# Optimization experiments

Measured on AMD Instinct MI355X. Metric: run time of the kernel, lower is better.

## Reference

```python
import jax, jax.numpy as jnp
import numpy as np

BIN_RES = 0.01
NUM_BINS = 512
T0 = 0.0
DECAY = 2.0
SCALE = 0.05
N = 131072


def setup_inputs() -> dict:
    key = jax.random.key(0)
    k1, k2, k3, k4, k5, k6 = jax.random.split(key, 6)
    means = jax.random.normal(k1, (N, 3), dtype=jnp.float32)
    scan_point = jax.random.normal(k2, (3,), dtype=jnp.float32)
    # parameters initialized near their nn.Parameter defaults with small noise
    colours = 0.1 + 0.05 * jax.random.normal(k3, (N, 1), dtype=jnp.float32)
    coefficients = 0.1 * jax.random.normal(k4, (N, 1), dtype=jnp.float32)
    opacities = 0.1 * jax.random.normal(k5, (N, 1), dtype=jnp.float32)
    pre_act_scales = jnp.log(jnp.float32(SCALE)) + 0.1 * jax.random.normal(k6, (N, 1), dtype=jnp.float32)
    return {
        "means": means,
        "scan_point": scan_point,
        "colours": colours,
        "coefficients": coefficients,
        "opacities": opacities,
        "pre_act_scales": pre_act_scales,
        "view_id": 0,
    }


def reference(means, scan_point, colours, coefficients, opacities, pre_act_scales, view_id):
    # render_conf_hist2 (confocal=True path)
    intensity = jax.nn.sigmoid(opacities[:, view_id]) * (colours[:, 0] ** 2)  # [N]
    coeff = jax.nn.sigmoid(coefficients)  # [N,1]
    r0 = jnp.linalg.norm(means - scan_point[None, :], axis=1, keepdims=True)  # [N,1]
    r_ = T0 / 2 + (BIN_RES / 2) * jnp.arange(1, 1 + NUM_BINS, dtype=jnp.float32)  # [B]
    r = r_[None, :]  # [1,B]
    sigma = jnp.mean(jnp.exp(pre_act_scales), axis=1, keepdims=True)  # [N,1]
    sigma = jnp.clip(sigma, BIN_RES / 2)  # lower clip only
    d = r - r0  # [N,B]
    g = jnp.exp(-0.5 * (d / sigma) ** 2)  # [N,B]
    pdf1 = np.sqrt(0.5 / np.pi) * g / sigma
    pdf2 = d * g / (sigma ** 2)
    pdf = coeff * pdf1 + (1.0 - coeff) * pdf2
    pr = jnp.clip(pdf * (BIN_RES / 2), 0.0, 1.0)  # [N,B]
    hist = jnp.sum(intensity[:, None] * pr, axis=0)  # [B]
    hist = hist / jnp.power(r_, DECAY)
    return hist
```

## Files before the change

### kernel.cpp

```cpp
#include <hip/hip_runtime.h>
#include <math.h>

#define NBINS 512
#define K1_THREADS 512

__global__ __launch_bounds__(K1_THREADS) void gauss_scatter_fused(
    const float* __restrict__ means,
    const float* __restrict__ scan_point,
    const float* __restrict__ colours,
    const float* __restrict__ coefficients,
    const float* __restrict__ opacities,
    const float* __restrict__ pre_act,
    const int*   __restrict__ view_id_p,
    float* __restrict__ out,
    int n)
{
    __shared__ float hist[NBINS];
    const int tid = threadIdx.x;
    hist[tid] = 0.0f;
    __syncthreads();

    const int i = blockIdx.x * K1_THREADS + tid;
    if (i < n) {
        const int vid = view_id_p[0];
        const float op  = opacities[i + vid];
        const float col = colours[i];
        const float inten = (1.0f / (1.0f + __expf(-op))) * col * col;
        const float cf    = 1.0f / (1.0f + __expf(-coefficients[i]));

        const float dx = means[3*i]   - scan_point[0];
        const float dy = means[3*i+1] - scan_point[1];
        const float dz = means[3*i+2] - scan_point[2];
        const float r0 = sqrtf(fmaf(dx, dx, fmaf(dy, dy, dz*dz)));

        const float sigma = fmaxf(__expf(pre_act[i]), 0.005f);

        const float q  = 0.8493218002880191f / sigma;
        const float c  = inten * 0.005f;
        const float A2 = c * cf * 0.3989422804014327f / sigma;
        const float B3 = c * (1.0f - cf) / (0.8493218002880191f * sigma);

        const float rlo = r0 - (cf / (1.0f - cf)) * 0.3989422804014327f * sigma;
        const float rhi = r0 + 7.5f * sigma;
        int blo = (int)ceilf(rlo * 200.0f - 1.0f);
        int bhi = (int)floorf(rhi * 200.0f - 1.0f);
        blo = max(blo, 0);
        bhi = min(bhi, NBINS - 1);

        float e = (0.005f * (float)(blo + 1) - r0) * q;
        const float de = 0.005f * q;
        for (int b = blo; b <= bhi; ++b) {
            const float g = __builtin_amdgcn_exp2f(-(e * e));
            const float t = g * fmaf(B3, e, A2);
            unsafeAtomicAdd(&hist[b], t);
            e += de;
        }
    }
    __syncthreads();

    const float v = hist[tid];
    if (v != 0.0f) {
        const float r = 0.005f * (float)(tid + 1);
        unsafeAtomicAdd(&out[tid], v / (r * r));
    }
}

extern "C" void kernel_launch(void* const* d_in, const int* in_sizes, int n_in,
                              void* d_out, int out_size, void* d_ws, size_t ws_size,
                              hipStream_t stream) {
    const float* means        = (const float*)d_in[0];
    const float* scan_point   = (const float*)d_in[1];
    const float* colours      = (const float*)d_in[2];
    const float* coefficients = (const float*)d_in[3];
    const float* opacities    = (const float*)d_in[4];
    const float* pre_act      = (const float*)d_in[5];
    const int*   view_id      = (const int*)d_in[6];

    const int n = in_sizes[2];
    const int G = (n + K1_THREADS - 1) / K1_THREADS;

    float* out = (float*)d_out;

    hipMemsetAsync(out, 0, NBINS * sizeof(float), stream);

    gauss_scatter_fused<<<G, K1_THREADS, 0, stream>>>(
        means, scan_point, colours, coefficients, opacities, pre_act,
        view_id, out, n);
}
```

Baseline: 23.63 us.

## Replace global atomics and memset with cooperative grid-sync reduction

Switches to a persistent cooperative launch of 256 blocks, each grid-striding over gaussians and accumulating into a shared histogram. Each block writes its partial histogram to workspace, then after a grid-wide sync the blocks reduce the partials per bin with wave shuffles. This removes the separate memset launch and the global atomic contention on the output. In exchange it adds a grid barrier, a workspace round trip, and the overhead of a cooperative launch.

```diff
diff --git a/kernel.cpp b/kernel.cpp
--- a/kernel.cpp
+++ b/kernel.cpp
@@ -1,10 +1,14 @@
 #include <hip/hip_runtime.h>
+#include <hip/hip_cooperative_groups.h>
 #include <math.h>
 
-#define NBINS 512
-#define K1_THREADS 512
+namespace cg = cooperative_groups;
 
-__global__ __launch_bounds__(K1_THREADS) void gauss_scatter_fused(
+#define NBINS  512
+#define TPB    512
+#define GBLKS  256
+
+__global__ __launch_bounds__(TPB) void gauss_fused_coop(
     const float* __restrict__ means,
     const float* __restrict__ scan_point,
     const float* __restrict__ colours,
@@ -12,6 +16,7 @@
     const float* __restrict__ opacities,
     const float* __restrict__ pre_act,
     const int*   __restrict__ view_id_p,
+    float* __restrict__ partial,
     float* __restrict__ out,
     int n)
 {
@@ -20,8 +25,7 @@
     hist[tid] = 0.0f;
     __syncthreads();
 
-    const int i = blockIdx.x * K1_THREADS + tid;
-    if (i < n) {
+    for (int i = blockIdx.x * TPB + tid; i < n; i += GBLKS * TPB) {
         const int vid = view_id_p[0];
         const float op  = opacities[i + vid];
         const float col = colours[i];
@@ -58,10 +62,28 @@
     }
     __syncthreads();
 
-    const float v = hist[tid];
-    if (v != 0.0f) {
+    {
         const float r = 0.005f * (float)(tid + 1);
-        unsafeAtomicAdd(&out[tid], v / (r * r));
+        partial[blockIdx.x * NBINS + tid] = hist[tid] / (r * r);
+    }
+    __threadfence();
+    cg::this_grid().sync();
+
+    const int half = tid >> 8;
+    const int bin  = blockIdx.x * 2 + half;
+    const int g    = tid & 255;
+    float s = partial[g * NBINS + bin];
+
+    #pragma unroll
+    for (int off = 32; off > 0; off >>= 1)
+        s += __shfl_down(s, off, 64);
+
+    __shared__ float wsum[8];
+    if ((tid & 63) == 0) wsum[tid >> 6] = s;
+    __syncthreads();
+    if ((tid & 255) == 0) {
+        const int base = half * 4;
+        out[bin] = wsum[base] + wsum[base + 1] + wsum[base + 2] + wsum[base + 3];
     }
 }
 
@@ -76,14 +98,15 @@
     const float* pre_act      = (const float*)d_in[5];
     const int*   view_id      = (const int*)d_in[6];
 
-    const int n = in_sizes[2];
-    const int G = (n + K1_THREADS - 1) / K1_THREADS;
+    int n = in_sizes[2];
+    float* partial = (float*)d_ws;
+    float* out     = (float*)d_out;
 
-    float* out = (float*)d_out;
-
-    hipMemsetAsync(out, 0, NBINS * sizeof(float), stream);
-
-    gauss_scatter_fused<<<G, K1_THREADS, 0, stream>>>(
-        means, scan_point, colours, coefficients, opacities, pre_act,
-        view_id, out, n);
+    void* args[] = {
+        (void*)&means, (void*)&scan_point, (void*)&colours,
+        (void*)&coefficients, (void*)&opacities, (void*)&pre_act,
+        (void*)&view_id, (void*)&partial, (void*)&out, (void*)&n
+    };
+    hipLaunchCooperativeKernel((const void*)gauss_fused_coop,
+                               dim3(GBLKS), dim3(TPB), args, 0, stream);
 }
```

New measurement: 85.38 us. 3.61x slower.

## Replace global atomics and memset with last-block reduction of per-block partials

Applied to the files above, without the earlier changes.

Each block writes its normalized histogram to a workspace partial buffer, and a global counter picks the last-arriving block, which sums all partials and writes the output directly. This drops the separate memset launch and the contended global atomic adds on the 512 output bins. In exchange it adds a serial reduction over 256 partial rows in a single block, plus reliance on a counter that is never reset, which works only through the modulo-G trick.

```diff
diff --git a/kernel.cpp b/kernel.cpp
--- a/kernel.cpp
+++ b/kernel.cpp
@@ -2,9 +2,9 @@
 #include <math.h>
 
 #define NBINS 512
-#define K1_THREADS 512
+#define TPB   512
 
-__global__ __launch_bounds__(K1_THREADS) void gauss_scatter_fused(
+__global__ __launch_bounds__(TPB) void gauss_onenode2(
     const float* __restrict__ means,
     const float* __restrict__ scan_point,
     const float* __restrict__ colours,
@@ -12,15 +12,19 @@
     const float* __restrict__ opacities,
     const float* __restrict__ pre_act,
     const int*   __restrict__ view_id_p,
+    float* __restrict__ partial,
+    unsigned int* __restrict__ counter,
     float* __restrict__ out,
-    int n)
+    int n, int G)
 {
     __shared__ float hist[NBINS];
+    __shared__ int s_last;
     const int tid = threadIdx.x;
+    const int bid = blockIdx.x;
     hist[tid] = 0.0f;
     __syncthreads();
 
-    const int i = blockIdx.x * K1_THREADS + tid;
+    const int i = bid * TPB + tid;
     if (i < n) {
         const int vid = view_id_p[0];
         const float op  = opacities[i + vid];
@@ -42,27 +46,46 @@
 
         const float rlo = r0 - (cf / (1.0f - cf)) * 0.3989422804014327f * sigma;
         const float rhi = r0 + 7.5f * sigma;
-        int blo = (int)ceilf(rlo * 200.0f - 1.0f);
-        int bhi = (int)floorf(rhi * 200.0f - 1.0f);
-        blo = max(blo, 0);
-        bhi = min(bhi, NBINS - 1);
+        int blo = max((int)ceilf(rlo * 200.0f - 1.0f), 0);
+        int bhi = min((int)floorf(rhi * 200.0f - 1.0f), NBINS - 1);
 
         float e = (0.005f * (float)(blo + 1) - r0) * q;
         const float de = 0.005f * q;
         for (int b = blo; b <= bhi; ++b) {
             const float g = __builtin_amdgcn_exp2f(-(e * e));
-            const float t = g * fmaf(B3, e, A2);
-            unsafeAtomicAdd(&hist[b], t);
+            unsafeAtomicAdd(&hist[b], g * fmaf(B3, e, A2));
             e += de;
         }
     }
     __syncthreads();
 
-    const float v = hist[tid];
-    if (v != 0.0f) {
+    {
         const float r = 0.005f * (float)(tid + 1);
-        unsafeAtomicAdd(&out[tid], v / (r * r));
+        __hip_atomic_store(&partial[bid * NBINS + tid], hist[tid] / (r * r),
+                           __ATOMIC_RELAXED, __HIP_MEMORY_SCOPE_AGENT);
     }
+
+    if (tid == 0) {
+        const unsigned int old = __hip_atomic_fetch_add(
+            counter, 1u, __ATOMIC_ACQ_REL, __HIP_MEMORY_SCOPE_AGENT);
+        s_last = (old % (unsigned)G) == (unsigned)(G - 1);
+    }
+    __syncthreads();
+    if (!s_last) return;
+
+    float s0 = 0.f, s1 = 0.f, s2 = 0.f, s3 = 0.f;
+    int g = 0;
+    #pragma unroll 8
+    for (; g + 3 < G; g += 4) {
+        s0 += __hip_atomic_load(&partial[(g    ) * NBINS + tid], __ATOMIC_RELAXED, __HIP_MEMORY_SCOPE_AGENT);
+        s1 += __hip_atomic_load(&partial[(g + 1) * NBINS + tid], __ATOMIC_RELAXED, __HIP_MEMORY_SCOPE_AGENT);
+        s2 += __hip_atomic_load(&partial[(g + 2) * NBINS + tid], __ATOMIC_RELAXED, __HIP_MEMORY_SCOPE_AGENT);
+        s3 += __hip_atomic_load(&partial[(g + 3) * NBINS + tid], __ATOMIC_RELAXED, __HIP_MEMORY_SCOPE_AGENT);
+    }
+    for (; g < G; ++g)
+        s0 += __hip_atomic_load(&partial[g * NBINS + tid], __ATOMIC_RELAXED, __HIP_MEMORY_SCOPE_AGENT);
+
+    out[tid] = (s0 + s1) + (s2 + s3);
 }
 
 extern "C" void kernel_launch(void* const* d_in, const int* in_sizes, int n_in,
@@ -77,13 +100,13 @@
     const int*   view_id      = (const int*)d_in[6];
 
     const int n = in_sizes[2];
-    const int G = (n + K1_THREADS - 1) / K1_THREADS;
+    const int G = (n + TPB - 1) / TPB;
 
-    float* out = (float*)d_out;
+    float*        partial = (float*)d_ws;
+    unsigned int* counter = (unsigned int*)((char*)d_ws + (size_t)G * NBINS * sizeof(float));
+    float*        out     = (float*)d_out;
 
-    hipMemsetAsync(out, 0, NBINS * sizeof(float), stream);
-
-    gauss_scatter_fused<<<G, K1_THREADS, 0, stream>>>(
+    gauss_onenode2<<<G, TPB, 0, stream>>>(
         means, scan_point, colours, coefficients, opacities, pre_act,
-        view_id, out, n);
+        view_id, partial, counter, out, n, G);
 }
```

New measurement: 35.91 us. +52.0%, slower.
